# Kernel optimization log

Hardware: AMD Instinct MI355X
Metric: run time of the kernel (lower is better)

Reference implementation:

```python
import jax, jax.numpy as jnp
import numpy as np

R = 4        # in_transformations == out_transformations
FS = 3       # filter_size
PAD = 1
STRIDE = 1


def setup_inputs() -> dict:
    key = jax.random.key(0)
    k1, k2, k3 = jax.random.split(key, 3)
    B, Cin, O, K = 16, 64, 64, 4
    Ctot = Cin * R  # 256
    x = jax.random.normal(k1, (B, Ctot, 64, 64), dtype=jnp.float32)
    # kernel bank: [num_dynamic_kernels, out_channels, in_channels, f, f]
    kernel_bank = jax.random.normal(k2, (K, O, Cin, FS, FS), dtype=jnp.float32) * 0.05
    # routing fc: Linear(total_in_channels -> num_kernels)
    fc_w = jax.random.normal(k3, (K, Ctot), dtype=jnp.float32) * 0.05
    fc_b = jnp.zeros((K,), dtype=jnp.float32)
    return {"x": x, "kernel_bank": kernel_bank, "fc_w": fc_w, "fc_b": fc_b}


def reference(x, kernel_bank, fc_w, fc_b):
    B, Ctot, H, W = x.shape
    K, O, Cin, f, _ = kernel_bank.shape
    # --- dynamic routing: global avg pool -> fc -> sigmoid ---
    pooled = x.mean(axis=(2, 3))                                  # [B, Ctot]
    coeffs = jax.nn.sigmoid(pooled @ fc_w.T + fc_b)               # [B, K]
    # --- per-sample kernel synthesis ---
    base = jnp.einsum('bk,kocij->bocij', coeffs, kernel_bank)     # [B, O, Cin, f, f]
    # rotations rot90^k for k in 0..R-1 (matches torch.rot90 dims=(-2,-1))
    rotated = jnp.stack([jnp.rot90(base, k, axes=(-2, -1)) for k in range(R)], axis=1)  # [B, R, O, Cin, f, f]
    # block kernel: block (r_out, r_in) uses rotation index (r_out - r_in) % R,
    # so the r_in sum of convs becomes one conv over all R*Cin input channels.
    r_out = jnp.arange(R)[:, None]
    r_in = jnp.arange(R)[None, :]
    idx = (r_out - r_in) % R                                      # [R, R]
    big = rotated[:, idx]                                         # [B, R_out, R_in, O, Cin, f, f]
    big = big.transpose(0, 1, 3, 2, 4, 5, 6).reshape(B, R * O, R * Cin, f, f)
    # --- per-sample conv (vmapped over batch; each sample has its own kernel) ---
    def conv_one(xi, wi):
        return jax.lax.conv_general_dilated(
            xi[None], wi,
            window_strides=(STRIDE, STRIDE),
            padding=[(PAD, PAD), (PAD, PAD)],
            dimension_numbers=('NCHW', 'OIHW', 'NCHW'))[0]
    return jax.vmap(conv_one)(x, big)                             # [B, R*O, H, W]
```

## Files before the change

### kernel.cpp

```cpp
#include <hip/hip_runtime.h>
#include <hip/hip_bf16.h>
#include <math.h>

#define BATCH 16
#define CT    256
#define HW    64
#define OCH   64
#define NK    4
#define HP    66

typedef __attribute__((ext_vector_type(4))) float  f32x4;
typedef __attribute__((ext_vector_type(8))) short  s16x8;
typedef __attribute__((ext_vector_type(4))) unsigned short u16x4;

#define GLOBAL_AS __attribute__((address_space(1)))
#define LDS_AS    __attribute__((address_space(3)))

__device__ __constant__ int c_rotsrc[4][9] = {
    {0,1,2,3,4,5,6,7,8},
    {2,5,8,1,4,7,0,3,6},
    {8,7,6,5,4,3,2,1,0},
    {6,3,0,7,4,1,8,5,2}
};

static __device__ inline unsigned short f2bf(float f) {
    union { __hip_bfloat16 h; unsigned short u; } cv;
    cv.h = __float2bfloat16(f);
    return cv.u;
}

__global__ __launch_bounds__(256) void xpose_pool(const float* __restrict__ x,
                                                  unsigned short* __restrict__ xT,
                                                  float* __restrict__ partial) {
    const int ci0 = blockIdx.x * 64;
    const int pr  = blockIdx.y;
    const int b   = blockIdx.z;
    const int t   = threadIdx.x;
    unsigned short* xrow = xT + ((size_t)(b*HP + pr))*HP*CT;

    if (pr == 0 || pr == HP-1) {
        for (int u = t; u < HP*16; u += 256) {
            int c = u >> 4, q = u & 15;
            *(u16x4*)(xrow + c*CT + ci0 + q*4) = (u16x4)0;
        }
        return;
    }
    const int r = pr - 1;

    __shared__ unsigned short tile[64][70];
    const int cilL = t >> 4;
    const int c0   = (t & 15) * 4;
    #pragma unroll
    for (int i = 0; i < 4; ++i) {
        int cil = cilL + i*16;
        (void)cil;
    }
    const int cilH = t >> 4;
    #pragma unroll
    for (int i = 0; i < 4; ++i) {
        int cil = cilH + i*16;
        f32x4 v = *(const f32x4*)(x + (((size_t)(b*CT + ci0 + cil))*HW + r)*HW + c0);
        tile[cil][c0+0] = f2bf(v[0]);
        tile[cil][c0+1] = f2bf(v[1]);
        tile[cil][c0+2] = f2bf(v[2]);
        tile[cil][c0+3] = f2bf(v[3]);
        float s = v[0] + v[1] + v[2] + v[3];
        s += __shfl_xor(s, 1, 16);
        s += __shfl_xor(s, 2, 16);
        s += __shfl_xor(s, 4, 16);
        s += __shfl_xor(s, 8, 16);
        if ((t & 15) == 0)
            partial[((size_t)(b*HW) + r)*CT + ci0 + cil] = s;
    }
    __syncthreads();

    if (t < 32) {
        int colp = (t >> 4) * (HP-1);
        int q    = t & 15;
        *(u16x4*)(xrow + colp*CT + ci0 + q*4) = (u16x4)0;
    }
    #pragma unroll
    for (int i = 0; i < 4; ++i) {
        int u = i*256 + t;
        int c = u >> 4, cil0 = (u & 15) * 4;
        u16x4 w;
        w[0] = tile[cil0+0][c];
        w[1] = tile[cil0+1][c];
        w[2] = tile[cil0+2][c];
        w[3] = tile[cil0+3][c];
        *(u16x4*)(xrow + (c+1)*CT + ci0 + cil0) = w;
    }
}

__global__ __launch_bounds__(256) void coeff_kernel(const float* __restrict__ partial,
                                                    const float* __restrict__ fc_w,
                                                    const float* __restrict__ fc_b,
                                                    float* __restrict__ coeffs) {
    const int b = blockIdx.x;
    const int t = threadIdx.x;
    const float* pp = partial + (size_t)b*HW*CT + t;
    float s = 0.f;
    #pragma unroll 8
    for (int r = 0; r < HW; ++r) s += pp[(size_t)r*CT];
    __shared__ float pool[CT];
    pool[t] = s * (1.f / (HW*HW));
    __syncthreads();
    const int w = t >> 6, l = t & 63;
    float d = 0.f;
    for (int c = l; c < CT; c += 64) d += pool[c] * fc_w[w*CT + c];
    for (int off = 32; off; off >>= 1) d += __shfl_down(d, off, 64);
    if (l == 0)
        coeffs[b*NK + w] = 1.f / (1.f + expf(-(d + fc_b[w])));
}

__global__ __launch_bounds__(256) void bankrot_kernel(const float* __restrict__ bank,
                                                      float* __restrict__ P) {
    const int idx = blockIdx.x * 256 + threadIdx.x;
    const int o = idx & 63;
    const int c = (idx >> 6) & 63;
    const int k = idx >> 12;
    const float* bp = bank + ((size_t)((k*OCH + o)*64 + c))*9;
    float v[9];
    #pragma unroll
    for (int s = 0; s < 9; ++s) v[s] = bp[s];
    #pragma unroll
    for (int rr = 0; rr < 4; ++rr)
        #pragma unroll
        for (int s = 0; s < 9; ++s)
            P[(size_t)(((k*4 + rr)*9 + s))*4096 + c*64 + o] = v[c_rotsrc[rr][s]];
}

__global__ __launch_bounds__(256) void wbuild_kernel(const float* __restrict__ coeffs,
                                                     const float* __restrict__ P,
                                                     unsigned short* __restrict__ Wb) {
    const int cig = blockIdx.x;
    const int s   = blockIdx.y;
    const int co  = threadIdx.x;
    const int ro  = co >> 6;
    const int o   = co & 63;
    const int ri  = cig >> 3;
    const int rr  = (ro - ri) & 3;
    const int c8  = (cig & 7) * 8;

    float r[NK][8];
    #pragma unroll
    for (int k = 0; k < NK; ++k) {
        const float* pp = P + (size_t)(((k*4 + rr)*9 + s))*4096 + o;
        #pragma unroll
        for (int q = 0; q < 8; ++q)
            r[k][q] = pp[(c8 + q)*64];
    }
    #pragma unroll
    for (int b = 0; b < BATCH; ++b) {
        const float cf0 = coeffs[b*NK+0], cf1 = coeffs[b*NK+1];
        const float cf2 = coeffs[b*NK+2], cf3 = coeffs[b*NK+3];
        s16x8 w;
        #pragma unroll
        for (int q = 0; q < 8; ++q) {
            float v = cf0*r[0][q] + cf1*r[1][q] + cf2*r[2][q] + cf3*r[3][q];
            w[q] = (short)f2bf(v);
        }
        *(s16x8*)(Wb + ((((size_t)(b*9 + s)*32 + cig)*256 + co) << 3)) = w;
    }
}

#define CHUNK_UNITS 1056
#define BUF_UNITS   1088
__global__ __launch_bounds__(256, 2) void conv_mfma(
        const unsigned short* __restrict__ xT,
        const unsigned short* __restrict__ Wb,
        float* __restrict__ out) {
    const int bid = blockIdx.x;
    const int xcd = bid & 7;
    const int sub = bid >> 3;
    const int b   = xcd*2 + (sub & 1);
    const int rt  = sub >> 1;
    const int r0  = rt * 2;

    const int t    = threadIdx.x;
    const int w    = t >> 6;
    const int lane = t & 63;
    const int lo16 = lane & 15;
    const int hi4  = lane >> 4;
    const int wco  = w & 1;
    const int wrow = w >> 1;
    const int co0  = wco * 128;

    __shared__ __align__(16) unsigned short Xs[2*BUF_UNITS*8];

    f32x4 acc[8][4];
    #pragma unroll
    for (int f = 0; f < 8; ++f)
        #pragma unroll
        for (int p = 0; p < 4; ++p)
            acc[f][p] = (f32x4)0.f;

#define STAGE(CH, BUF)                                                          \
    do {                                                                        \
        const int ci0_ = (CH) * 32;                                             \
        _Pragma("unroll")                                                       \
        for (int it = 0; it < 5; ++it) {                                        \
            int ubase = it*256 + w*64;                                          \
            if (ubase < CHUNK_UNITS) {                                          \
                int u  = ubase + lane;                                          \
                int us = u > (CHUNK_UNITS-1) ? (CHUNK_UNITS-1) : u;             \
                int pl = us >> 2, q = us & 3;                                   \
                int rr = pl / 66, cc = pl - rr*66;                              \
                const unsigned short* src = xT +                                \
                    (((size_t)(b*HP + r0 + rr))*HP + cc)*CT + ci0_ + q*8;       \
                __builtin_amdgcn_global_load_lds(                               \
                    (const GLOBAL_AS void*)src,                                 \
                    (LDS_AS void*)(Xs + (size_t)((BUF)*BUF_UNITS + ubase)*8),   \
                    16, 0, 0);                                                  \
            }                                                                   \
        }                                                                       \
    } while (0)

    STAGE(0, 0);

    for (int ch = 0; ch < 8; ++ch) {
        __syncthreads();
        if (ch < 7) STAGE(ch+1, (ch+1) & 1);
        const int bufoff = (ch & 1) * (BUF_UNITS*16);

        #pragma unroll
        for (int s = 0; s < 9; ++s) {
            const int dr = s / 3, dc = s % 3;
            const unsigned short* wp = Wb +
                ((((size_t)(b*9 + s)*32) + ch*4 + hi4)*256 + co0 + lo16)*8;
            s16x8 a0 = *(const s16x8*)(wp + 0*128);
            s16x8 a1 = *(const s16x8*)(wp + 1*128);
            s16x8 a2 = *(const s16x8*)(wp + 2*128);
            s16x8 a3 = *(const s16x8*)(wp + 3*128);
            s16x8 a4 = *(const s16x8*)(wp + 4*128);
            s16x8 a5 = *(const s16x8*)(wp + 5*128);
            s16x8 a6 = *(const s16x8*)(wp + 6*128);
            s16x8 a7 = *(const s16x8*)(wp + 7*128);
            const int pbase = bufoff + ((wrow + dr)*66 + dc + lo16)*64 + hi4*16;
            #pragma unroll
            for (int cf = 0; cf < 4; ++cf) {
                s16x8 bf = *(const s16x8*)((const char*)Xs + pbase + cf*1024);
                acc[0][cf] = __builtin_amdgcn_mfma_f32_16x16x32_bf16(a0, bf, acc[0][cf], 0, 0, 0);
                acc[1][cf] = __builtin_amdgcn_mfma_f32_16x16x32_bf16(a1, bf, acc[1][cf], 0, 0, 0);
                acc[2][cf] = __builtin_amdgcn_mfma_f32_16x16x32_bf16(a2, bf, acc[2][cf], 0, 0, 0);
                acc[3][cf] = __builtin_amdgcn_mfma_f32_16x16x32_bf16(a3, bf, acc[3][cf], 0, 0, 0);
                acc[4][cf] = __builtin_amdgcn_mfma_f32_16x16x32_bf16(a4, bf, acc[4][cf], 0, 0, 0);
                acc[5][cf] = __builtin_amdgcn_mfma_f32_16x16x32_bf16(a5, bf, acc[5][cf], 0, 0, 0);
                acc[6][cf] = __builtin_amdgcn_mfma_f32_16x16x32_bf16(a6, bf, acc[6][cf], 0, 0, 0);
                acc[7][cf] = __builtin_amdgcn_mfma_f32_16x16x32_bf16(a7, bf, acc[7][cf], 0, 0, 0);
            }
        }
    }
#undef STAGE

    const int prow = r0 + wrow;
    #pragma unroll
    for (int f = 0; f < 8; ++f)
        #pragma unroll
        for (int cf = 0; cf < 4; ++cf)
            #pragma unroll
            for (int j = 0; j < 4; ++j) {
                int co = co0 + f*16 + hi4*4 + j;
                out[(((size_t)(b*CT + co))*HW + prow)*HW + cf*16 + lo16] =
                    acc[f][cf][j];
            }
}

extern "C" void kernel_launch(void* const* d_in, const int* in_sizes, int n_in,
                              void* d_out, int out_size, void* d_ws, size_t ws_size,
                              hipStream_t stream) {
    const float* x    = (const float*)d_in[0];
    const float* bank = (const float*)d_in[1];
    const float* fc_w = (const float*)d_in[2];
    const float* fc_b = (const float*)d_in[3];
    float* out = (float*)d_out;

    char* wsb = (char*)d_ws;
    float* partial = (float*)wsb;
    float* Prot    = (float*)wsb;
    float* coeffs  = (float*)(wsb + 2359296);
    unsigned short* Wb = (unsigned short*)(wsb + 2360320);
    unsigned short* xT = (unsigned short*)(wsb + 21234688);

    xpose_pool<<<dim3(4, HP, BATCH), 256, 0, stream>>>(x, xT, partial);
    coeff_kernel<<<BATCH, 256, 0, stream>>>(partial, fc_w, fc_b, coeffs);
    bankrot_kernel<<<64, 256, 0, stream>>>(bank, Prot);
    wbuild_kernel<<<dim3(32, 9), 256, 0, stream>>>(coeffs, Prot, Wb);
    conv_mfma<<<512, 256, 0, stream>>>(xT, Wb, out);
}
```

Measured before the change: 104.3 us.

## Regroup activation layout into 8-channel planes and split waves by output channels

The transposed bf16 activation buffer changes from pixel-major with all 256 channels interleaved to channel-group-major planes (8 channels per 16-byte unit, padded 66x66 plane). Staging loads therefore read contiguous pixel runs per channel group. The conv kernel's wave split changes from 2 output-channel halves x 2 rows to 4 output-channel quarters each covering both rows. Each wave now holds 4 weight fragments and 8 pixel fragments instead of 8 and 4, which reduces per-wave weight loads from global memory but doubles LDS B-fragment reads.

Measured after the change: 100.2 us. 4.0% less time.

```diff
diff --git a/kernel.cpp b/kernel.cpp
--- a/kernel.cpp
+++ b/kernel.cpp
@@ -8,6 +8,7 @@
 #define OCH   64
 #define NK    4
 #define HP    66
+#define NPIX  4356
 
 typedef __attribute__((ext_vector_type(4))) float  f32x4;
 typedef __attribute__((ext_vector_type(8))) short  s16x8;
@@ -30,32 +31,27 @@
 }
 
 __global__ __launch_bounds__(256) void xpose_pool(const float* __restrict__ x,
-                                                  unsigned short* __restrict__ xT,
+                                                  unsigned short* __restrict__ xTg,
                                                   float* __restrict__ partial) {
     const int ci0 = blockIdx.x * 64;
+    const int g0  = ci0 >> 3;
     const int pr  = blockIdx.y;
     const int b   = blockIdx.z;
     const int t   = threadIdx.x;
-    unsigned short* xrow = xT + ((size_t)(b*HP + pr))*HP*CT;
 
     if (pr == 0 || pr == HP-1) {
-        for (int u = t; u < HP*16; u += 256) {
-            int c = u >> 4, q = u & 15;
-            *(u16x4*)(xrow + c*CT + ci0 + q*4) = (u16x4)0;
+        for (int u = t; u < 8*HP; u += 256) {
+            int g = u / HP, c = u % HP;
+            *(s16x8*)(xTg + ((((size_t)(b*32 + g0 + g))*NPIX) + pr*HP + c)*8) =
+                (s16x8)(short)0;
         }
         return;
     }
     const int r = pr - 1;
 
     __shared__ unsigned short tile[64][70];
-    const int cilL = t >> 4;
+    const int cilH = t >> 4;
     const int c0   = (t & 15) * 4;
-    #pragma unroll
-    for (int i = 0; i < 4; ++i) {
-        int cil = cilL + i*16;
-        (void)cil;
-    }
-    const int cilH = t >> 4;
     #pragma unroll
     for (int i = 0; i < 4; ++i) {
         int cil = cilH + i*16;
@@ -74,21 +70,22 @@
     }
     __syncthreads();
 
-    if (t < 32) {
-        int colp = (t >> 4) * (HP-1);
-        int q    = t & 15;
-        *(u16x4*)(xrow + colp*CT + ci0 + q*4) = (u16x4)0;
+    if (t < 16) {
+        int g = t & 7, side = t >> 3;
+        *(s16x8*)(xTg + ((((size_t)(b*32 + g0 + g))*NPIX) + pr*HP + side*(HP-1))*8) =
+            (s16x8)(short)0;
     }
     #pragma unroll
     for (int i = 0; i < 4; ++i) {
         int u = i*256 + t;
-        int c = u >> 4, cil0 = (u & 15) * 4;
+        int c = u & 63, cil0 = (u >> 6) * 4;
         u16x4 w;
         w[0] = tile[cil0+0][c];
         w[1] = tile[cil0+1][c];
         w[2] = tile[cil0+2][c];
         w[3] = tile[cil0+3][c];
-        *(u16x4*)(xrow + (c+1)*CT + ci0 + cil0) = w;
+        *(u16x4*)(xTg + ((((size_t)(b*32 + g0 + (cil0>>3)))*NPIX) + pr*HP + c + 1)*8
+                  + (cil0 & 4)) = w;
     }
 }
 
@@ -167,14 +164,12 @@
 #define CHUNK_UNITS 1056
 #define BUF_UNITS   1088
 __global__ __launch_bounds__(256, 2) void conv_mfma(
-        const unsigned short* __restrict__ xT,
+        const unsigned short* __restrict__ xTg,
         const unsigned short* __restrict__ Wb,
         float* __restrict__ out) {
     const int bid = blockIdx.x;
-    const int xcd = bid & 7;
-    const int sub = bid >> 3;
-    const int b   = xcd*2 + (sub & 1);
-    const int rt  = sub >> 1;
+    const int b   = (bid & 7)*2 + ((bid >> 3) & 1);
+    const int rt  = bid >> 4;
     const int r0  = rt * 2;
 
     const int t    = threadIdx.x;
@@ -182,32 +177,28 @@
     const int lane = t & 63;
     const int lo16 = lane & 15;
     const int hi4  = lane >> 4;
-    const int wco  = w & 1;
-    const int wrow = w >> 1;
-    const int co0  = wco * 128;
 
     __shared__ __align__(16) unsigned short Xs[2*BUF_UNITS*8];
 
-    f32x4 acc[8][4];
-    #pragma unroll
-    for (int f = 0; f < 8; ++f)
-        #pragma unroll
-        for (int p = 0; p < 4; ++p)
+    f32x4 acc[4][8];
+    #pragma unroll
+    for (int f = 0; f < 4; ++f)
+        #pragma unroll
+        for (int p = 0; p < 8; ++p)
             acc[f][p] = (f32x4)0.f;
 
 #define STAGE(CH, BUF)                                                          \
     do {                                                                        \
-        const int ci0_ = (CH) * 32;                                             \
         _Pragma("unroll")                                                       \
         for (int it = 0; it < 5; ++it) {                                        \
             int ubase = it*256 + w*64;                                          \
             if (ubase < CHUNK_UNITS) {                                          \
                 int u  = ubase + lane;                                          \
                 int us = u > (CHUNK_UNITS-1) ? (CHUNK_UNITS-1) : u;             \
-                int pl = us >> 2, q = us & 3;                                   \
-                int rr = pl / 66, cc = pl - rr*66;                              \
-                const unsigned short* src = xT +                                \
-                    (((size_t)(b*HP + r0 + rr))*HP + cc)*CT + ci0_ + q*8;       \
+                int q  = us / 264;                                              \
+                int pl = us - q*264;                                            \
+                const unsigned short* src = xTg +                               \
+                    (((size_t)(b*32 + (CH)*4 + q))*NPIX + r0*HP + pl)*8;        \
                 __builtin_amdgcn_global_load_lds(                               \
                     (const GLOBAL_AS void*)src,                                 \
                     (LDS_AS void*)(Xs + (size_t)((BUF)*BUF_UNITS + ubase)*8),   \
@@ -221,49 +212,43 @@
     for (int ch = 0; ch < 8; ++ch) {
         __syncthreads();
         if (ch < 7) STAGE(ch+1, (ch+1) & 1);
-        const int bufoff = (ch & 1) * (BUF_UNITS*16);
+        const char* Xb = (const char*)Xs + (ch & 1)*(BUF_UNITS*16)
+                         + hi4*(264*16) + lo16*16;
 
         #pragma unroll
         for (int s = 0; s < 9; ++s) {
             const int dr = s / 3, dc = s % 3;
             const unsigned short* wp = Wb +
-                ((((size_t)(b*9 + s)*32) + ch*4 + hi4)*256 + co0 + lo16)*8;
+                ((((size_t)(b*9 + s)*32) + ch*4 + hi4)*256 + w*64 + lo16)*8;
             s16x8 a0 = *(const s16x8*)(wp + 0*128);
             s16x8 a1 = *(const s16x8*)(wp + 1*128);
             s16x8 a2 = *(const s16x8*)(wp + 2*128);
             s16x8 a3 = *(const s16x8*)(wp + 3*128);
-            s16x8 a4 = *(const s16x8*)(wp + 4*128);
-            s16x8 a5 = *(const s16x8*)(wp + 5*128);
-            s16x8 a6 = *(const s16x8*)(wp + 6*128);
-            s16x8 a7 = *(const s16x8*)(wp + 7*128);
-            const int pbase = bufoff + ((wrow + dr)*66 + dc + lo16)*64 + hi4*16;
             #pragma unroll
-            for (int cf = 0; cf < 4; ++cf) {
-                s16x8 bf = *(const s16x8*)((const char*)Xs + pbase + cf*1024);
-                acc[0][cf] = __builtin_amdgcn_mfma_f32_16x16x32_bf16(a0, bf, acc[0][cf], 0, 0, 0);
-                acc[1][cf] = __builtin_amdgcn_mfma_f32_16x16x32_bf16(a1, bf, acc[1][cf], 0, 0, 0);
-                acc[2][cf] = __builtin_amdgcn_mfma_f32_16x16x32_bf16(a2, bf, acc[2][cf], 0, 0, 0);
-                acc[3][cf] = __builtin_amdgcn_mfma_f32_16x16x32_bf16(a3, bf, acc[3][cf], 0, 0, 0);
-                acc[4][cf] = __builtin_amdgcn_mfma_f32_16x16x32_bf16(a4, bf, acc[4][cf], 0, 0, 0);
-                acc[5][cf] = __builtin_amdgcn_mfma_f32_16x16x32_bf16(a5, bf, acc[5][cf], 0, 0, 0);
-                acc[6][cf] = __builtin_amdgcn_mfma_f32_16x16x32_bf16(a6, bf, acc[6][cf], 0, 0, 0);
-                acc[7][cf] = __builtin_amdgcn_mfma_f32_16x16x32_bf16(a7, bf, acc[7][cf], 0, 0, 0);
+            for (int p = 0; p < 8; ++p) {
+                const int pixbase = ((p >> 2) + dr)*HP + dc + (p & 3)*16;
+                s16x8 bf = *(const s16x8*)(Xb + pixbase*16);
+                acc[0][p] = __builtin_amdgcn_mfma_f32_16x16x32_bf16(a0, bf, acc[0][p], 0, 0, 0);
+                acc[1][p] = __builtin_amdgcn_mfma_f32_16x16x32_bf16(a1, bf, acc[1][p], 0, 0, 0);
+                acc[2][p] = __builtin_amdgcn_mfma_f32_16x16x32_bf16(a2, bf, acc[2][p], 0, 0, 0);
+                acc[3][p] = __builtin_amdgcn_mfma_f32_16x16x32_bf16(a3, bf, acc[3][p], 0, 0, 0);
             }
         }
     }
 #undef STAGE
 
-    const int prow = r0 + wrow;
-    #pragma unroll
-    for (int f = 0; f < 8; ++f)
-        #pragma unroll
-        for (int cf = 0; cf < 4; ++cf)
+    #pragma unroll
+    for (int f = 0; f < 4; ++f)
+        #pragma unroll
+        for (int p = 0; p < 8; ++p) {
+            const int row = r0 + (p >> 2);
+            const int colb = (p & 3)*16 + lo16;
             #pragma unroll
             for (int j = 0; j < 4; ++j) {
-                int co = co0 + f*16 + hi4*4 + j;
-                out[(((size_t)(b*CT + co))*HW + prow)*HW + cf*16 + lo16] =
-                    acc[f][cf][j];
+                int co = w*64 + f*16 + hi4*4 + j;
+                out[(((size_t)(b*CT + co))*HW + row)*HW + colb] = acc[f][p][j];
             }
+        }
 }
 
 extern "C" void kernel_launch(void* const* d_in, const int* in_sizes, int n_in,
@@ -279,12 +264,12 @@
     float* partial = (float*)wsb;
     float* Prot    = (float*)wsb;
     float* coeffs  = (float*)(wsb + 2359296);
-    unsigned short* Wb = (unsigned short*)(wsb + 2360320);
-    unsigned short* xT = (unsigned short*)(wsb + 21234688);
-
-    xpose_pool<<<dim3(4, HP, BATCH), 256, 0, stream>>>(x, xT, partial);
+    unsigned short* Wb  = (unsigned short*)(wsb + 2360320);
+    unsigned short* xTg = (unsigned short*)(wsb + 21234688);
+
+    xpose_pool<<<dim3(4, HP, BATCH), 256, 0, stream>>>(x, xTg, partial);
     coeff_kernel<<<BATCH, 256, 0, stream>>>(partial, fc_w, fc_b, coeffs);
     bankrot_kernel<<<64, 256, 0, stream>>>(bank, Prot);
     wbuild_kernel<<<dim3(32, 9), 256, 0, stream>>>(coeffs, Prot, Wb);
-    conv_mfma<<<512, 256, 0, stream>>>(xT, Wb, out);
-}
+    conv_mfma<<<512, 256, 0, stream>>>(xTg, Wb, out);
+}
```
